# Optimization experiments

Measured on AMD Instinct MI355X. Metric: run time of the kernel, lower is better.

The kernel has to match this reference:

```python
import jax, jax.numpy as jnp
import numpy as np
import math

B, T, D_MODEL, H = 2, 2048, 768, 12
D = D_MODEL // H
EPS = 1e-8


def _l2norm(x, eps=EPS):
    # torch.nn.functional.normalize: x / max(||x||, eps)
    n = jnp.sqrt(jnp.sum(x * x, axis=-1, keepdims=True))
    return x / jnp.maximum(n, eps)


def setup_inputs() -> dict:
    key = jax.random.key(0)
    ks = jax.random.split(key, 7)
    sc = 1.0 / math.sqrt(D_MODEL)
    inp = {
        "query": jax.random.normal(ks[0], (B, T, D_MODEL), jnp.float32),
        "key": jax.random.normal(ks[1], (B, T, D_MODEL), jnp.float32),
        "value": jax.random.normal(ks[2], (B, T, D_MODEL), jnp.float32),
        "Wq": jax.random.normal(ks[3], (D_MODEL, D_MODEL), jnp.float32) * sc,
        "Wk": jax.random.normal(ks[4], (D_MODEL, D_MODEL), jnp.float32) * sc,
        "Wv": jax.random.normal(ks[5], (D_MODEL, D_MODEL), jnp.float32) * sc,
        "Wo": jax.random.normal(ks[6], (D_MODEL, D_MODEL), jnp.float32) * sc,
        "s_v": jnp.linspace(0.0, math.log(255.0), H).astype(jnp.float32),
        "s_r": jnp.zeros((H,), jnp.float32),
    }
    return inp


def reference(query, key, value, Wq, Wk, Wv, Wo, s_v, s_r):
    b, t, _ = query.shape

    def proj(x, W):  # Linear(bias=False) then split heads -> [B,H,T,D]
        return (x @ W.T).reshape(b, t, H, D).transpose(0, 2, 1, 3)

    q = _l2norm(proj(query, Wq))
    k = _l2norm(proj(key, Wk))
    v = _l2norm(proj(value, Wv))

    w = jnp.exp(s_v) + 1.0  # per-head decay exponent, in [2, 256]
    r = jnp.exp(s_r) + 1.0  # per-head scale

    # cosine-similarity scores in [-1, 1]
    s = jnp.einsum("bhqd,bhkd->bhqk", q, k)
    base = jnp.clip((s + 1.0) * 0.5, 0.0, 1.0)
    alpha = r[None, :, None, None] * jnp.power(base, w[None, :, None, None])

    # causal mask (no softmax normalization in screening attention)
    causal = jnp.tril(jnp.ones((t, t), dtype=bool))
    alpha = jnp.where(causal[None, None], alpha, 0.0)

    out = jnp.einsum("bhqk,bhkd->bhqd", alpha, v)  # [B,H,T,D]

    # TanhNorm: bound magnitude along head dim via tanh of the norm
    n = jnp.sqrt(jnp.sum(out * out, axis=-1, keepdims=True))
    out = jnp.tanh(n) * out / (n + EPS)

    out = out.transpose(0, 2, 1, 3).reshape(b, t, D_MODEL)
    return out @ Wo.T
```

## Files before the change

kernel.cpp:

```cpp
#include <hip/hip_runtime.h>
#include <hip/hip_bf16.h>
#include <math.h>


typedef __attribute__((ext_vector_type(8))) short short8;
typedef __attribute__((ext_vector_type(4))) float f32x4;
typedef __attribute__((ext_vector_type(4))) unsigned int uint4v;
typedef __attribute__((ext_vector_type(2))) unsigned int uint2v;
typedef __attribute__((ext_vector_type(4))) float float4v;

#define MFMA_BF16(a, b, c) __builtin_amdgcn_mfma_f32_16x16x32_bf16((a), (b), (c), 0, 0, 0)

static __device__ __forceinline__ unsigned short f2bf(float f) {
  union { float f; unsigned u; } v; v.f = f;
  unsigned r = v.u + 0x7FFFu + ((v.u >> 16) & 1u);
  return (unsigned short)(r >> 16);
}
static __device__ __forceinline__ unsigned pack2(float a, float b) {
  return (unsigned)f2bf(a) | ((unsigned)f2bf(b) << 16);
}
static __device__ __forceinline__ void gload_lds16(const void* g, void* l) {
  __builtin_amdgcn_global_load_lds((const __attribute__((address_space(1))) unsigned int*)g,
                                   (__attribute__((address_space(3))) unsigned int*)l, 16, 0, 0);
}

__global__ __launch_bounds__(256) void k_cvt(
    const float* __restrict__ s0, const float* __restrict__ s1, const float* __restrict__ s2,
    const float* __restrict__ s3, const float* __restrict__ s4, const float* __restrict__ s5,
    const float* __restrict__ s6, unsigned short* __restrict__ dst) {
  const size_t e = ((size_t)blockIdx.x * 256 + threadIdx.x) * 8;
  const float* src;
  size_t off;
  if (e < 9437184) {
    const int i = (int)(e / 3145728);
    src = (i == 0) ? s0 : (i == 1) ? s1 : s2;
    off = e - (size_t)i * 3145728;
  } else {
    const size_t ew = e - 9437184;
    const int i = (int)(ew / 589824);
    src = (i == 0) ? s3 : (i == 1) ? s4 : (i == 2) ? s5 : s6;
    off = ew - (size_t)i * 589824;
  }
  const float4v f0 = *(const float4v*)(src + off);
  const float4v f1 = *(const float4v*)(src + off + 4);
  uint4v u = {pack2(f0.x, f0.y), pack2(f0.z, f0.w), pack2(f1.x, f1.y), pack2(f1.z, f1.w)};
  *(uint4v*)(dst + e) = u;
}

__global__ __launch_bounds__(256) void k_proj(
    const unsigned short* __restrict__ Xb, const unsigned short* __restrict__ Wb,
    unsigned short* __restrict__ qb, unsigned short* __restrict__ kb,
    unsigned short* __restrict__ vtb) {
  __shared__ alignas(16) unsigned char smem[65536];
  float* o_s = (float*)smem;
  unsigned short* vt_s = (unsigned short*)smem;

  const int which = blockIdx.z;
  const unsigned short* X = Xb + (size_t)which * 3145728;
  const unsigned short* W = Wb + (size_t)which * 589824;

  const int mbase = blockIdx.x * 128;
  const int nb = blockIdx.y;
  const int tid = threadIdx.x;
  const int lane = tid & 63;
  const int wv = tid >> 6;
  const int wm = wv >> 1, wn = wv & 1;
  const int l15 = lane & 15, l4 = lane >> 4;

  const int srow8 = lane >> 3;
  const int schunk = (lane & 7) ^ srow8;

  f32x4 acc[4][4];
#pragma unroll
  for (int m = 0; m < 4; ++m)
#pragma unroll
    for (int n = 0; n < 4; ++n) acc[m][n] = (f32x4){0.f, 0.f, 0.f, 0.f};

#pragma unroll
  for (int i = 0; i < 4; ++i) {
    const int j = wv * 4 + i;
    gload_lds16(X + (size_t)(mbase + j * 8 + srow8) * 768 + schunk * 8, smem + j * 1024);
    gload_lds16(W + (size_t)(nb * 128 + j * 8 + srow8) * 768 + schunk * 8,
                smem + 16384 + j * 1024);
  }

  for (int ks = 0; ks < 12; ++ks) {
    const int cur = (ks & 1) * 32768;
    asm volatile("s_waitcnt vmcnt(0)" ::: "memory");
    __builtin_amdgcn_sched_barrier(0);
    __builtin_amdgcn_s_barrier();
    __builtin_amdgcn_sched_barrier(0);
    if (ks < 11) {
      const int nxt = ((ks + 1) & 1) * 32768;
      const int k0n = (ks + 1) * 64;
#pragma unroll
      for (int i = 0; i < 4; ++i) {
        const int j = wv * 4 + i;
        gload_lds16(X + (size_t)(mbase + j * 8 + srow8) * 768 + k0n + schunk * 8,
                    smem + nxt + j * 1024);
        gload_lds16(W + (size_t)(nb * 128 + j * 8 + srow8) * 768 + k0n + schunk * 8,
                    smem + nxt + 16384 + j * 1024);
      }
      __builtin_amdgcn_sched_barrier(0);
    }
    __builtin_amdgcn_s_setprio(1);
#pragma unroll
    for (int kc = 0; kc < 2; ++kc) {
      const int cx = (kc << 2) | l4;
      short8 ar[4], br[4];
#pragma unroll
      for (int m = 0; m < 4; ++m) {
        const int r = wm * 64 + m * 16 + l15;
        ar[m] = *(const short8*)(smem + cur + r * 128 + ((cx ^ (r & 7)) << 4));
      }
#pragma unroll
      for (int n = 0; n < 4; ++n) {
        const int r = wn * 64 + n * 16 + l15;
        br[n] = *(const short8*)(smem + cur + 16384 + r * 128 + ((cx ^ (r & 7)) << 4));
      }
#pragma unroll
      for (int m = 0; m < 4; ++m)
#pragma unroll
        for (int n = 0; n < 4; ++n) acc[m][n] = MFMA_BF16(ar[m], br[n], acc[m][n]);
    }
    __builtin_amdgcn_s_setprio(0);
  }

  const int b = mbase >> 11;
  const int tbase = mbase & 2047;
  const int row2 = tid >> 1, half = tid & 1;
  for (int p = 0; p < 2; ++p) {
    __syncthreads();
    if (wn == p) {
#pragma unroll
      for (int m = 0; m < 4; ++m)
#pragma unroll
        for (int n = 0; n < 4; ++n)
#pragma unroll
          for (int j = 0; j < 4; ++j)
            o_s[(wm * 64 + m * 16 + l4 * 4 + j) * 68 + n * 16 + l15] = acc[m][n][j];
    }
    __syncthreads();
    float v[32];
    float ss = 0.f;
#pragma unroll
    for (int c = 0; c < 8; ++c) {
      float4v f = *(const float4v*)(o_s + row2 * 68 + half * 32 + c * 4);
      v[c * 4 + 0] = f.x; v[c * 4 + 1] = f.y; v[c * 4 + 2] = f.z; v[c * 4 + 3] = f.w;
      ss += f.x * f.x + f.y * f.y + f.z * f.z + f.w * f.w;
    }
    ss += __shfl_xor(ss, 1);
    const float inv = 1.f / fmaxf(sqrtf(ss), 1e-8f);
    const int h = nb * 2 + p, bh = b * 12 + h;
    if (which < 2) {
      unsigned short* outp =
          ((which == 0) ? qb : kb) + ((size_t)bh * 2048 + tbase + row2) * 64 + half * 32;
#pragma unroll
      for (int c = 0; c < 4; ++c) {
        uint4v o = {pack2(v[c * 8 + 0] * inv, v[c * 8 + 1] * inv),
                    pack2(v[c * 8 + 2] * inv, v[c * 8 + 3] * inv),
                    pack2(v[c * 8 + 4] * inv, v[c * 8 + 5] * inv),
                    pack2(v[c * 8 + 6] * inv, v[c * 8 + 7] * inv)};
        *(uint4v*)(outp + c * 8) = o;
      }
      __syncthreads();
    } else {
      __syncthreads();
#pragma unroll
      for (int c = 0; c < 32; ++c)
        vt_s[(half * 32 + c) * 136 + row2] = f2bf(v[c] * inv);
      __syncthreads();
      const int d = tid >> 2, tc = (tid & 3) * 32;
      unsigned short* dst = vtb + ((size_t)bh * 64 + d) * 2048 + tbase + tc;
#pragma unroll
      for (int c = 0; c < 4; ++c)
        *(uint4v*)(dst + c * 8) = *(const uint4v*)(vt_s + d * 136 + tc + c * 8);
      __syncthreads();
    }
  }
}

__global__ __launch_bounds__(256) void k_attn(
    const unsigned short* __restrict__ qb, const unsigned short* __restrict__ kb,
    const unsigned short* __restrict__ vtb, const float* __restrict__ s_v,
    const float* __restrict__ s_r, unsigned short* __restrict__ attn) {
  __shared__ alignas(16) unsigned char smem[41984];
  unsigned short* p_s = (unsigned short*)(smem + 32768);
  float* o_s = (float*)smem;

  const int bid = blockIdx.x;
  const int ii = bid & 255, jj = bid >> 8;
  const int rank = (jj == 0) ? ii : (jj == 1) ? (511 - ii) : (512 + ii);
  const int qt = 31 - (rank / 24);
  const int bh = rank % 24;
  const int b = bh / 12, h = bh % 12;
  const int qbase = qt * 64;
  const unsigned short* Qp = qb + (size_t)bh * 2048 * 64;
  const unsigned short* Kp = kb + (size_t)bh * 2048 * 64;
  const unsigned short* VTp = vtb + (size_t)bh * 64 * 2048;

  const int tid = threadIdx.x;
  const int lane = tid & 63;
  const int wv = tid >> 6;
  const int wm = wv >> 1, wn = wv & 1;
  const int l15 = lane & 15, l4 = lane >> 4;
  const int srow8 = lane >> 3;
  const int schunk = (lane & 7) ^ srow8;

  const float w_h = expf(s_v[h]) + 1.0f;
  const float lr_h = log2f(expf(s_r[h]) + 1.0f);

#pragma unroll
  for (int i = 0; i < 2; ++i) {
    const int j = wv * 2 + i;
    gload_lds16(Kp + (size_t)(j * 8 + srow8) * 64 + schunk * 8, smem + j * 1024);
    gload_lds16(VTp + (size_t)(j * 8 + srow8) * 2048 + schunk * 8, smem + 16384 + j * 1024);
  }

  short8 qf[2][2];
#pragma unroll
  for (int n = 0; n < 2; ++n)
#pragma unroll
    for (int kc = 0; kc < 2; ++kc)
      qf[n][kc] = *(const short8*)(Qp + (size_t)(qbase + wn * 32 + n * 16 + l15) * 64 + kc * 32 +
                                   l4 * 8);

  f32x4 acc_o[2][2];
#pragma unroll
  for (int m = 0; m < 2; ++m)
#pragma unroll
    for (int n = 0; n < 2; ++n) acc_o[m][n] = (f32x4){0.f, 0.f, 0.f, 0.f};

  for (int kt = 0; kt <= qt; ++kt) {
    const int cur = (kt & 1) * 8192;
    asm volatile("s_waitcnt vmcnt(0)" ::: "memory");
    __builtin_amdgcn_sched_barrier(0);
    __builtin_amdgcn_s_barrier();
    __builtin_amdgcn_sched_barrier(0);
    if (kt < qt) {
      const int nxt = ((kt + 1) & 1) * 8192;
      const int kb2 = (kt + 1) * 64;
#pragma unroll
      for (int i = 0; i < 2; ++i) {
        const int j = wv * 2 + i;
        gload_lds16(Kp + (size_t)(kb2 + j * 8 + srow8) * 64 + schunk * 8, smem + nxt + j * 1024);
        gload_lds16(VTp + (size_t)(j * 8 + srow8) * 2048 + kb2 + schunk * 8,
                    smem + 16384 + nxt + j * 1024);
      }
      __builtin_amdgcn_sched_barrier(0);
    }
    f32x4 s_acc[2][2];
#pragma unroll
    for (int m = 0; m < 2; ++m)
#pragma unroll
      for (int n = 0; n < 2; ++n) s_acc[m][n] = (f32x4){0.f, 0.f, 0.f, 0.f};
    __builtin_amdgcn_s_setprio(1);
#pragma unroll
    for (int kc = 0; kc < 2; ++kc) {
      const int cx = (kc << 2) | l4;
      const int r0 = wm * 32 + l15, r1 = wm * 32 + 16 + l15;
      short8 a0 = *(const short8*)(smem + cur + r0 * 128 + ((cx ^ (r0 & 7)) << 4));
      short8 a1 = *(const short8*)(smem + cur + r1 * 128 + ((cx ^ (r1 & 7)) << 4));
      s_acc[0][0] = MFMA_BF16(a0, qf[0][kc], s_acc[0][0]);
      s_acc[0][1] = MFMA_BF16(a0, qf[1][kc], s_acc[0][1]);
      s_acc[1][0] = MFMA_BF16(a1, qf[0][kc], s_acc[1][0]);
      s_acc[1][1] = MFMA_BF16(a1, qf[1][kc], s_acc[1][1]);
    }
    __builtin_amdgcn_s_setprio(0);
    const bool diag = (kt == qt);
#pragma unroll
    for (int m = 0; m < 2; ++m)
#pragma unroll
      for (int n = 0; n < 2; ++n) {
        const int lkb = wm * 32 + m * 16 + l4 * 4;
        const int lq = wn * 32 + n * 16 + l15;
        float av[4];
#pragma unroll
        for (int t = 0; t < 4; ++t) {
          const float base = __builtin_amdgcn_fmed3f(fmaf(s_acc[m][n][t], 0.5f, 0.5f), 0.f, 1.f);
          float a = __builtin_amdgcn_exp2f(fmaf(w_h, __builtin_amdgcn_logf(base), lr_h));
          if (diag && (lkb + t) > lq) a = 0.f;
          av[t] = a;
        }
        uint2v u = {pack2(av[0], av[1]), pack2(av[2], av[3])};
        *(uint2v*)(p_s + lq * 72 + lkb) = u;
      }
    asm volatile("s_waitcnt lgkmcnt(0)" ::: "memory");
    __builtin_amdgcn_sched_barrier(0);
    __builtin_amdgcn_s_barrier();
    __builtin_amdgcn_sched_barrier(0);
    __builtin_amdgcn_s_setprio(1);
#pragma unroll
    for (int kc = 0; kc < 2; ++kc) {
      const int cx = (kc << 2) | l4;
      const int r0 = wm * 32 + l15, r1 = wm * 32 + 16 + l15;
      short8 pa0 = *(const short8*)(p_s + (wn * 32 + l15) * 72 + kc * 32 + l4 * 8);
      short8 pa1 = *(const short8*)(p_s + (wn * 32 + 16 + l15) * 72 + kc * 32 + l4 * 8);
      short8 vb0 = *(const short8*)(smem + 16384 + cur + r0 * 128 + ((cx ^ (r0 & 7)) << 4));
      short8 vb1 = *(const short8*)(smem + 16384 + cur + r1 * 128 + ((cx ^ (r1 & 7)) << 4));
      acc_o[0][0] = MFMA_BF16(pa0, vb0, acc_o[0][0]);
      acc_o[0][1] = MFMA_BF16(pa0, vb1, acc_o[0][1]);
      acc_o[1][0] = MFMA_BF16(pa1, vb0, acc_o[1][0]);
      acc_o[1][1] = MFMA_BF16(pa1, vb1, acc_o[1][1]);
    }
    __builtin_amdgcn_s_setprio(0);
  }
  __syncthreads();
#pragma unroll
  for (int qi = 0; qi < 2; ++qi)
#pragma unroll
    for (int di = 0; di < 2; ++di)
#pragma unroll
      for (int j = 0; j < 4; ++j)
        o_s[(wn * 32 + qi * 16 + l4 * 4 + j) * 68 + wm * 32 + di * 16 + l15] = acc_o[qi][di][j];
  __syncthreads();
  {
    const int row = tid >> 2, q4 = tid & 3;
    float vals[16];
    float ss = 0.f;
#pragma unroll
    for (int j = 0; j < 16; ++j) {
      vals[j] = o_s[row * 68 + q4 * 16 + j];
      ss += vals[j] * vals[j];
    }
    ss += __shfl_xor(ss, 1);
    ss += __shfl_xor(ss, 2);
    const float nrm = sqrtf(ss);
    const float sc = tanhf(nrm) / (nrm + 1e-8f);
    unsigned short* dst = attn + (size_t)(b * 2048 + qbase + row) * 768 + h * 64 + q4 * 16;
    uint4v o0 = {pack2(vals[0] * sc, vals[1] * sc), pack2(vals[2] * sc, vals[3] * sc),
                 pack2(vals[4] * sc, vals[5] * sc), pack2(vals[6] * sc, vals[7] * sc)};
    uint4v o1 = {pack2(vals[8] * sc, vals[9] * sc), pack2(vals[10] * sc, vals[11] * sc),
                 pack2(vals[12] * sc, vals[13] * sc), pack2(vals[14] * sc, vals[15] * sc)};
    *(uint4v*)(dst) = o0;
    *(uint4v*)(dst + 8) = o1;
  }
}

__global__ __launch_bounds__(256) void k_outproj(const unsigned short* __restrict__ attn,
                                                 const unsigned short* __restrict__ Wob,
                                                 float* __restrict__ out) {
  __shared__ alignas(16) unsigned char smem[65536];
  const int mbase = blockIdx.x * 128;
  const int nb = blockIdx.y;
  const int tid = threadIdx.x;
  const int lane = tid & 63;
  const int wv = tid >> 6;
  const int wm = wv >> 1, wn = wv & 1;
  const int l15 = lane & 15, l4 = lane >> 4;
  const int srow8 = lane >> 3;
  const int schunk = (lane & 7) ^ srow8;

  f32x4 acc[4][4];
#pragma unroll
  for (int m = 0; m < 4; ++m)
#pragma unroll
    for (int n = 0; n < 4; ++n) acc[m][n] = (f32x4){0.f, 0.f, 0.f, 0.f};

#pragma unroll
  for (int i = 0; i < 4; ++i) {
    const int j = wv * 4 + i;
    gload_lds16(attn + (size_t)(mbase + j * 8 + srow8) * 768 + schunk * 8, smem + j * 1024);
    gload_lds16(Wob + (size_t)(nb * 128 + j * 8 + srow8) * 768 + schunk * 8,
                smem + 16384 + j * 1024);
  }

  for (int ks = 0; ks < 12; ++ks) {
    const int cur = (ks & 1) * 32768;
    asm volatile("s_waitcnt vmcnt(0)" ::: "memory");
    __builtin_amdgcn_sched_barrier(0);
    __builtin_amdgcn_s_barrier();
    __builtin_amdgcn_sched_barrier(0);
    if (ks < 11) {
      const int nxt = ((ks + 1) & 1) * 32768;
      const int k0n = (ks + 1) * 64;
#pragma unroll
      for (int i = 0; i < 4; ++i) {
        const int j = wv * 4 + i;
        gload_lds16(attn + (size_t)(mbase + j * 8 + srow8) * 768 + k0n + schunk * 8,
                    smem + nxt + j * 1024);
        gload_lds16(Wob + (size_t)(nb * 128 + j * 8 + srow8) * 768 + k0n + schunk * 8,
                    smem + nxt + 16384 + j * 1024);
      }
      __builtin_amdgcn_sched_barrier(0);
    }
    __builtin_amdgcn_s_setprio(1);
#pragma unroll
    for (int kc = 0; kc < 2; ++kc) {
      const int cx = (kc << 2) | l4;
      short8 ar[4], br[4];
#pragma unroll
      for (int m = 0; m < 4; ++m) {
        const int r = wm * 64 + m * 16 + l15;
        ar[m] = *(const short8*)(smem + cur + r * 128 + ((cx ^ (r & 7)) << 4));
      }
#pragma unroll
      for (int n = 0; n < 4; ++n) {
        const int r = wn * 64 + n * 16 + l15;
        br[n] = *(const short8*)(smem + cur + 16384 + r * 128 + ((cx ^ (r & 7)) << 4));
      }
#pragma unroll
      for (int m = 0; m < 4; ++m)
#pragma unroll
        for (int n = 0; n < 4; ++n) acc[m][n] = MFMA_BF16(ar[m], br[n], acc[m][n]);
    }
    __builtin_amdgcn_s_setprio(0);
  }
#pragma unroll
  for (int m = 0; m < 4; ++m)
#pragma unroll
    for (int n = 0; n < 4; ++n)
#pragma unroll
      for (int j = 0; j < 4; ++j)
        out[(size_t)(mbase + wm * 64 + m * 16 + l4 * 4 + j) * 768 + nb * 128 + wn * 64 + n * 16 +
            l15] = acc[m][n][j];
}

extern "C" void kernel_launch(void* const* d_in, const int* in_sizes, int n_in, void* d_out,
                              int out_size, void* d_ws, size_t ws_size, hipStream_t stream) {
  (void)in_sizes;
  (void)n_in;
  (void)out_size;
  (void)ws_size;
  const float* query = (const float*)d_in[0];
  const float* key = (const float*)d_in[1];
  const float* value = (const float*)d_in[2];
  const float* Wq = (const float*)d_in[3];
  const float* Wk = (const float*)d_in[4];
  const float* Wv = (const float*)d_in[5];
  const float* Wo = (const float*)d_in[6];
  const float* s_v = (const float*)d_in[7];
  const float* s_r = (const float*)d_in[8];
  float* out = (float*)d_out;

  unsigned short* cvt = (unsigned short*)d_ws;
  unsigned short* Xb = cvt;
  unsigned short* Wb = cvt + 9437184;
  unsigned short* qb = cvt + 11796480;
  unsigned short* kb = qb + 3145728;
  unsigned short* vtb = kb + 3145728;
  unsigned short* attn = cvt;

  k_cvt<<<5760, 256, 0, stream>>>(query, key, value, Wq, Wk, Wv, Wo, cvt);
  k_proj<<<dim3(32, 6, 3), 256, 0, stream>>>(Xb, Wb, qb, kb, vtb);
  k_attn<<<dim3(768), 256, 0, stream>>>(qb, kb, vtb, s_v, s_r, attn);
  k_outproj<<<dim3(32, 6), 256, 0, stream>>>(attn, Wb + 3 * 589824, out);
}
```

Before: 89.53 us.

## Fuse fp32-to-bf16 activation conversion into projection GEMM A-tile loads

Stops converting the query/key/value activations in a separate pass. The projection kernel now loads the fp32 activations into registers, packs them to bf16 and writes them into the swizzled LDS tile, while the weights still arrive through async global-to-LDS loads. This removes a full write and read of the bf16 activation copy and shrinks the conversion kernel to weights only. In exchange it adds register pressure, ALU packing work and an LDS store plus lgkmcnt wait on the GEMM critical path, and each output-column block re-reads twice the activation bytes from global memory.

```diff
diff --git a/kernel.cpp b/kernel.cpp
--- a/kernel.cpp
+++ b/kernel.cpp
@@ -24,23 +24,13 @@
                                    (__attribute__((address_space(3))) unsigned int*)l, 16, 0, 0);
 }
 
-__global__ __launch_bounds__(256) void k_cvt(
-    const float* __restrict__ s0, const float* __restrict__ s1, const float* __restrict__ s2,
+__global__ __launch_bounds__(256) void k_cvtW(
     const float* __restrict__ s3, const float* __restrict__ s4, const float* __restrict__ s5,
     const float* __restrict__ s6, unsigned short* __restrict__ dst) {
   const size_t e = ((size_t)blockIdx.x * 256 + threadIdx.x) * 8;
-  const float* src;
-  size_t off;
-  if (e < 9437184) {
-    const int i = (int)(e / 3145728);
-    src = (i == 0) ? s0 : (i == 1) ? s1 : s2;
-    off = e - (size_t)i * 3145728;
-  } else {
-    const size_t ew = e - 9437184;
-    const int i = (int)(ew / 589824);
-    src = (i == 0) ? s3 : (i == 1) ? s4 : (i == 2) ? s5 : s6;
-    off = ew - (size_t)i * 589824;
-  }
+  const int i = (int)(e / 589824);
+  const float* src = (i == 0) ? s3 : (i == 1) ? s4 : (i == 2) ? s5 : s6;
+  const size_t off = e - (size_t)i * 589824;
   const float4v f0 = *(const float4v*)(src + off);
   const float4v f1 = *(const float4v*)(src + off + 4);
   uint4v u = {pack2(f0.x, f0.y), pack2(f0.z, f0.w), pack2(f1.x, f1.y), pack2(f1.z, f1.w)};
@@ -48,15 +38,15 @@
 }
 
 __global__ __launch_bounds__(256) void k_proj(
-    const unsigned short* __restrict__ Xb, const unsigned short* __restrict__ Wb,
-    unsigned short* __restrict__ qb, unsigned short* __restrict__ kb,
-    unsigned short* __restrict__ vtb) {
+    const float* __restrict__ Xq, const float* __restrict__ Xk, const float* __restrict__ Xv,
+    const unsigned short* __restrict__ Wb, unsigned short* __restrict__ qb,
+    unsigned short* __restrict__ kb, unsigned short* __restrict__ vtb) {
   __shared__ alignas(16) unsigned char smem[65536];
   float* o_s = (float*)smem;
   unsigned short* vt_s = (unsigned short*)smem;
 
   const int which = blockIdx.z;
-  const unsigned short* X = Xb + (size_t)which * 3145728;
+  const float* X = (which == 0) ? Xq : (which == 1) ? Xk : Xv;
   const unsigned short* W = Wb + (size_t)which * 589824;
 
   const int mbase = blockIdx.x * 128;
@@ -76,10 +66,21 @@
 #pragma unroll
     for (int n = 0; n < 4; ++n) acc[m][n] = (f32x4){0.f, 0.f, 0.f, 0.f};
 
+  const float* asrc[4];
+#pragma unroll
+  for (int i = 0; i < 4; ++i)
+    asrc[i] = X + (size_t)(mbase + (wv * 4 + i) * 8 + srow8) * 768 + schunk * 8;
+
+  float4v af[4][2];
+
+#pragma unroll
+  for (int i = 0; i < 4; ++i) {
+    af[i][0] = *(const float4v*)(asrc[i]);
+    af[i][1] = *(const float4v*)(asrc[i] + 4);
+  }
 #pragma unroll
   for (int i = 0; i < 4; ++i) {
     const int j = wv * 4 + i;
-    gload_lds16(X + (size_t)(mbase + j * 8 + srow8) * 768 + schunk * 8, smem + j * 1024);
     gload_lds16(W + (size_t)(nb * 128 + j * 8 + srow8) * 768 + schunk * 8,
                 smem + 16384 + j * 1024);
   }
@@ -88,16 +89,28 @@
     const int cur = (ks & 1) * 32768;
     asm volatile("s_waitcnt vmcnt(0)" ::: "memory");
     __builtin_amdgcn_sched_barrier(0);
+#pragma unroll
+    for (int i = 0; i < 4; ++i) {
+      uint4v u = {pack2(af[i][0].x, af[i][0].y), pack2(af[i][0].z, af[i][0].w),
+                  pack2(af[i][1].x, af[i][1].y), pack2(af[i][1].z, af[i][1].w)};
+      *(uint4v*)(smem + cur + (wv * 4 + i) * 1024 + lane * 16) = u;
+    }
+    __builtin_amdgcn_sched_barrier(0);
+    asm volatile("s_waitcnt lgkmcnt(0)" ::: "memory");
+    __builtin_amdgcn_sched_barrier(0);
     __builtin_amdgcn_s_barrier();
     __builtin_amdgcn_sched_barrier(0);
     if (ks < 11) {
+      const int k0n = (ks + 1) * 64;
       const int nxt = ((ks + 1) & 1) * 32768;
-      const int k0n = (ks + 1) * 64;
+#pragma unroll
+      for (int i = 0; i < 4; ++i) {
+        af[i][0] = *(const float4v*)(asrc[i] + k0n);
+        af[i][1] = *(const float4v*)(asrc[i] + k0n + 4);
+      }
 #pragma unroll
       for (int i = 0; i < 4; ++i) {
         const int j = wv * 4 + i;
-        gload_lds16(X + (size_t)(mbase + j * 8 + srow8) * 768 + k0n + schunk * 8,
-                    smem + nxt + j * 1024);
         gload_lds16(W + (size_t)(nb * 128 + j * 8 + srow8) * 768 + k0n + schunk * 8,
                     smem + nxt + 16384 + j * 1024);
       }
@@ -433,16 +446,14 @@
   const float* s_r = (const float*)d_in[8];
   float* out = (float*)d_out;
 
-  unsigned short* cvt = (unsigned short*)d_ws;
-  unsigned short* Xb = cvt;
-  unsigned short* Wb = cvt + 9437184;
-  unsigned short* qb = cvt + 11796480;
+  unsigned short* Wb = (unsigned short*)d_ws;
+  unsigned short* qb = Wb + 2359296;
   unsigned short* kb = qb + 3145728;
   unsigned short* vtb = kb + 3145728;
-  unsigned short* attn = cvt;
-
-  k_cvt<<<5760, 256, 0, stream>>>(query, key, value, Wq, Wk, Wv, Wo, cvt);
-  k_proj<<<dim3(32, 6, 3), 256, 0, stream>>>(Xb, Wb, qb, kb, vtb);
+  unsigned short* attn = vtb + 3145728;
+
+  k_cvtW<<<1152, 256, 0, stream>>>(Wq, Wk, Wv, Wo, Wb);
+  k_proj<<<dim3(32, 6, 3), 256, 0, stream>>>(query, key, value, Wb, qb, kb, vtb);
   k_attn<<<dim3(768), 256, 0, stream>>>(qb, kb, vtb, s_v, s_r, attn);
   k_outproj<<<dim3(32, 6), 256, 0, stream>>>(attn, Wb + 3 * 589824, out);
 }
```

Result: slower. 91.78 us (+2.5%).

## Stream-K split of causal attention tiles with partial sums and separate tanh-norm kernel

Applied to the files above, without the earlier changes.

Flattens all (head, query-tile, key-tile) causal work items into a linear sequence and gives each of the 768 blocks an equal contiguous strip of 16 or 17 tiles. A strip can cross query-tile and head boundaries, so each block writes fp32 partial accumulators into per-slot buffers instead of finishing rows itself. A new reduction kernel sums the partials, applies the TanhNorm and writes bf16 output. This targets load imbalance from triangular causal work, at the cost of extra fp32 partial traffic, an extra launch, and re-loading Q fragments at row changes.

```diff
diff --git a/kernel.cpp b/kernel.cpp
--- a/kernel.cpp
+++ b/kernel.cpp
@@ -22,6 +22,12 @@
 static __device__ __forceinline__ void gload_lds16(const void* g, void* l) {
   __builtin_amdgcn_global_load_lds((const __attribute__((address_space(1))) unsigned int*)g,
                                    (__attribute__((address_space(3))) unsigned int*)l, 16, 0, 0);
+}
+static __device__ __forceinline__ int strip_first(int s) {
+  return (s < 384) ? s * 17 : 6528 + (s - 384) * 16;
+}
+static __device__ __forceinline__ int strip_of(int g) {
+  return (g < 6528) ? g / 17 : 384 + (g - 6528) / 16;
 }
 
 __global__ __launch_bounds__(256) void k_cvt(
@@ -66,7 +72,6 @@
   const int wv = tid >> 6;
   const int wm = wv >> 1, wn = wv & 1;
   const int l15 = lane & 15, l4 = lane >> 4;
-
   const int srow8 = lane >> 3;
   const int schunk = (lane & 7) ^ srow8;
 
@@ -183,21 +188,20 @@
 __global__ __launch_bounds__(256) void k_attn(
     const unsigned short* __restrict__ qb, const unsigned short* __restrict__ kb,
     const unsigned short* __restrict__ vtb, const float* __restrict__ s_v,
-    const float* __restrict__ s_r, unsigned short* __restrict__ attn) {
+    const float* __restrict__ s_r, float* __restrict__ partials) {
   __shared__ alignas(16) unsigned char smem[41984];
   unsigned short* p_s = (unsigned short*)(smem + 32768);
-  float* o_s = (float*)smem;
-
-  const int bid = blockIdx.x;
-  const int ii = bid & 255, jj = bid >> 8;
-  const int rank = (jj == 0) ? ii : (jj == 1) ? (511 - ii) : (512 + ii);
-  const int qt = 31 - (rank / 24);
-  const int bh = rank % 24;
-  const int b = bh / 12, h = bh % 12;
-  const int qbase = qt * 64;
-  const unsigned short* Qp = qb + (size_t)bh * 2048 * 64;
-  const unsigned short* Kp = kb + (size_t)bh * 2048 * 64;
-  const unsigned short* VTp = vtb + (size_t)bh * 64 * 2048;
+
+  const int s = blockIdx.x;
+  const int gs = strip_first(s);
+  const int ge = strip_first(s + 1);
+
+  int bh = gs / 528;
+  int ii = gs - bh * 528;
+  int qt = (int)((sqrtf(8.f * (float)ii + 1.f) - 1.f) * 0.5f);
+  while ((qt + 1) * (qt + 2) / 2 <= ii) ++qt;
+  while (qt * (qt + 1) / 2 > ii) --qt;
+  int kt = ii - qt * (qt + 1) / 2;
 
   const int tid = threadIdx.x;
   const int lane = tid & 63;
@@ -207,23 +211,32 @@
   const int srow8 = lane >> 3;
   const int schunk = (lane & 7) ^ srow8;
 
-  const float w_h = expf(s_v[h]) + 1.0f;
-  const float lr_h = log2f(expf(s_r[h]) + 1.0f);
-
-#pragma unroll
-  for (int i = 0; i < 2; ++i) {
-    const int j = wv * 2 + i;
-    gload_lds16(Kp + (size_t)(j * 8 + srow8) * 64 + schunk * 8, smem + j * 1024);
-    gload_lds16(VTp + (size_t)(j * 8 + srow8) * 2048 + schunk * 8, smem + 16384 + j * 1024);
-  }
-
+  {
+    const unsigned short* Kp = kb + (size_t)bh * 131072;
+    const unsigned short* VTp = vtb + (size_t)bh * 131072;
+    const int kbase = kt * 64;
+#pragma unroll
+    for (int i = 0; i < 2; ++i) {
+      const int j = wv * 2 + i;
+      gload_lds16(Kp + (size_t)(kbase + j * 8 + srow8) * 64 + schunk * 8, smem + j * 1024);
+      gload_lds16(VTp + (size_t)(j * 8 + srow8) * 2048 + kbase + schunk * 8,
+                  smem + 16384 + j * 1024);
+    }
+  }
+
+  float w_h = expf(s_v[bh % 12]) + 1.0f;
+  float lr_h = log2f(expf(s_r[bh % 12]) + 1.0f);
   short8 qf[2][2];
-#pragma unroll
-  for (int n = 0; n < 2; ++n)
-#pragma unroll
-    for (int kc = 0; kc < 2; ++kc)
-      qf[n][kc] = *(const short8*)(Qp + (size_t)(qbase + wn * 32 + n * 16 + l15) * 64 + kc * 32 +
-                                   l4 * 8);
+  {
+    const unsigned short* Qp = qb + (size_t)bh * 131072;
+    const int qbase = qt * 64;
+#pragma unroll
+    for (int n = 0; n < 2; ++n)
+#pragma unroll
+      for (int kc = 0; kc < 2; ++kc)
+        qf[n][kc] = *(const short8*)(Qp + (size_t)(qbase + wn * 32 + n * 16 + l15) * 64 +
+                                     kc * 32 + l4 * 8);
+  }
 
   f32x4 acc_o[2][2];
 #pragma unroll
@@ -231,20 +244,29 @@
 #pragma unroll
     for (int n = 0; n < 2; ++n) acc_o[m][n] = (f32x4){0.f, 0.f, 0.f, 0.f};
 
-  for (int kt = 0; kt <= qt; ++kt) {
-    const int cur = (kt & 1) * 8192;
+  for (int g = gs; g < ge; ++g) {
+    const int cur = ((g - gs) & 1) * 8192;
+    const int qbase = qt * 64;
     asm volatile("s_waitcnt vmcnt(0)" ::: "memory");
     __builtin_amdgcn_sched_barrier(0);
     __builtin_amdgcn_s_barrier();
     __builtin_amdgcn_sched_barrier(0);
-    if (kt < qt) {
-      const int nxt = ((kt + 1) & 1) * 8192;
-      const int kb2 = (kt + 1) * 64;
+    int bh2 = bh, qt2 = qt, kt2 = kt + 1;
+    if (kt2 > qt2) {
+      kt2 = 0;
+      ++qt2;
+      if (qt2 == 32) { qt2 = 0; ++bh2; }
+    }
+    if (g + 1 < ge) {
+      const int nxt = ((g + 1 - gs) & 1) * 8192;
+      const unsigned short* Kp2 = kb + (size_t)bh2 * 131072;
+      const unsigned short* VTp2 = vtb + (size_t)bh2 * 131072;
+      const int kb2 = kt2 * 64;
 #pragma unroll
       for (int i = 0; i < 2; ++i) {
         const int j = wv * 2 + i;
-        gload_lds16(Kp + (size_t)(kb2 + j * 8 + srow8) * 64 + schunk * 8, smem + nxt + j * 1024);
-        gload_lds16(VTp + (size_t)(j * 8 + srow8) * 2048 + kb2 + schunk * 8,
+        gload_lds16(Kp2 + (size_t)(kb2 + j * 8 + srow8) * 64 + schunk * 8, smem + nxt + j * 1024);
+        gload_lds16(VTp2 + (size_t)(j * 8 + srow8) * 2048 + kb2 + schunk * 8,
                     smem + 16384 + nxt + j * 1024);
       }
       __builtin_amdgcn_sched_barrier(0);
@@ -304,37 +326,80 @@
       acc_o[1][1] = MFMA_BF16(pa1, vb1, acc_o[1][1]);
     }
     __builtin_amdgcn_s_setprio(0);
-  }
-  __syncthreads();
-#pragma unroll
-  for (int qi = 0; qi < 2; ++qi)
-#pragma unroll
-    for (int di = 0; di < 2; ++di)
-#pragma unroll
-      for (int j = 0; j < 4; ++j)
-        o_s[(wn * 32 + qi * 16 + l4 * 4 + j) * 68 + wm * 32 + di * 16 + l15] = acc_o[qi][di][j];
-  __syncthreads();
-  {
-    const int row = tid >> 2, q4 = tid & 3;
-    float vals[16];
-    float ss = 0.f;
-#pragma unroll
-    for (int j = 0; j < 16; ++j) {
-      vals[j] = o_s[row * 68 + q4 * 16 + j];
-      ss += vals[j] * vals[j];
-    }
-    ss += __shfl_xor(ss, 1);
-    ss += __shfl_xor(ss, 2);
-    const float nrm = sqrtf(ss);
-    const float sc = tanhf(nrm) / (nrm + 1e-8f);
-    unsigned short* dst = attn + (size_t)(b * 2048 + qbase + row) * 768 + h * 64 + q4 * 16;
-    uint4v o0 = {pack2(vals[0] * sc, vals[1] * sc), pack2(vals[2] * sc, vals[3] * sc),
-                 pack2(vals[4] * sc, vals[5] * sc), pack2(vals[6] * sc, vals[7] * sc)};
-    uint4v o1 = {pack2(vals[8] * sc, vals[9] * sc), pack2(vals[10] * sc, vals[11] * sc),
-                 pack2(vals[12] * sc, vals[13] * sc), pack2(vals[14] * sc, vals[15] * sc)};
-    *(uint4v*)(dst) = o0;
-    *(uint4v*)(dst + 8) = o1;
-  }
+    if (diag || (g + 1 == ge)) {
+      const int g0 = bh * 528 + qt * (qt + 1) / 2;
+      const int slot = s - strip_of(g0);
+      float* pb = partials + (((size_t)slot * 24 + bh) * 2048 + qbase) * 64;
+#pragma unroll
+      for (int qi = 0; qi < 2; ++qi)
+#pragma unroll
+        for (int di = 0; di < 2; ++di)
+#pragma unroll
+          for (int j = 0; j < 4; ++j)
+            pb[(size_t)(wn * 32 + qi * 16 + l4 * 4 + j) * 64 + wm * 32 + di * 16 + l15] =
+                acc_o[qi][di][j];
+#pragma unroll
+      for (int m = 0; m < 2; ++m)
+#pragma unroll
+        for (int n = 0; n < 2; ++n) acc_o[m][n] = (f32x4){0.f, 0.f, 0.f, 0.f};
+      if (g + 1 < ge) {
+        if (bh2 != bh) {
+          w_h = expf(s_v[bh2 % 12]) + 1.0f;
+          lr_h = log2f(expf(s_r[bh2 % 12]) + 1.0f);
+        }
+        const unsigned short* Qp2 = qb + (size_t)bh2 * 131072;
+        const int qbase2 = qt2 * 64;
+#pragma unroll
+        for (int n = 0; n < 2; ++n)
+#pragma unroll
+          for (int kc = 0; kc < 2; ++kc)
+            qf[n][kc] = *(const short8*)(Qp2 + (size_t)(qbase2 + wn * 32 + n * 16 + l15) * 64 +
+                                         kc * 32 + l4 * 8);
+      }
+    }
+    bh = bh2; qt = qt2; kt = kt2;
+  }
+}
+
+__global__ __launch_bounds__(256) void k_tanh(const float* __restrict__ partials,
+                                              unsigned short* __restrict__ attn) {
+  const int tid = threadIdx.x;
+  const int rg = blockIdx.x * 64 + (tid >> 2);
+  const int q4 = tid & 3;
+  const int bh = rg >> 11, t = rg & 2047;
+  const int qt = t >> 6;
+  const int g0 = bh * 528 + qt * (qt + 1) / 2;
+  const int cnt = strip_of(g0 + qt) - strip_of(g0) + 1;
+  float v[16];
+  const float* b0 = partials + ((size_t)bh * 2048 + t) * 64 + q4 * 16;
+#pragma unroll
+  for (int c = 0; c < 4; ++c) {
+    float4v f = *(const float4v*)(b0 + c * 4);
+    v[c * 4 + 0] = f.x; v[c * 4 + 1] = f.y; v[c * 4 + 2] = f.z; v[c * 4 + 3] = f.w;
+  }
+  for (int p = 1; p < cnt; ++p) {
+    const float* bp = b0 + (size_t)p * 3145728;
+#pragma unroll
+    for (int c = 0; c < 4; ++c) {
+      float4v f = *(const float4v*)(bp + c * 4);
+      v[c * 4 + 0] += f.x; v[c * 4 + 1] += f.y; v[c * 4 + 2] += f.z; v[c * 4 + 3] += f.w;
+    }
+  }
+  float ss = 0.f;
+#pragma unroll
+  for (int j = 0; j < 16; ++j) ss += v[j] * v[j];
+  ss += __shfl_xor(ss, 1);
+  ss += __shfl_xor(ss, 2);
+  const float nrm = sqrtf(ss);
+  const float sc = tanhf(nrm) / (nrm + 1e-8f);
+  unsigned short* dst =
+      attn + ((size_t)((bh / 12) * 2048 + t)) * 768 + (bh % 12) * 64 + q4 * 16;
+  uint4v o0 = {pack2(v[0] * sc, v[1] * sc), pack2(v[2] * sc, v[3] * sc),
+               pack2(v[4] * sc, v[5] * sc), pack2(v[6] * sc, v[7] * sc)};
+  uint4v o1 = {pack2(v[8] * sc, v[9] * sc), pack2(v[10] * sc, v[11] * sc),
+               pack2(v[12] * sc, v[13] * sc), pack2(v[14] * sc, v[15] * sc)};
+  *(uint4v*)(dst) = o0;
+  *(uint4v*)(dst + 8) = o1;
 }
 
 __global__ __launch_bounds__(256) void k_outproj(const unsigned short* __restrict__ attn,
@@ -439,10 +504,12 @@
   unsigned short* qb = cvt + 11796480;
   unsigned short* kb = qb + 3145728;
   unsigned short* vtb = kb + 3145728;
+  float* partials = (float*)(cvt + 21233664);
   unsigned short* attn = cvt;
 
   k_cvt<<<5760, 256, 0, stream>>>(query, key, value, Wq, Wk, Wv, Wo, cvt);
   k_proj<<<dim3(32, 6, 3), 256, 0, stream>>>(Xb, Wb, qb, kb, vtb);
-  k_attn<<<dim3(768), 256, 0, stream>>>(qb, kb, vtb, s_v, s_r, attn);
+  k_attn<<<dim3(768), 256, 0, stream>>>(qb, kb, vtb, s_v, s_r, partials);
+  k_tanh<<<dim3(768), 256, 0, stream>>>(partials, attn);
   k_outproj<<<dim3(32, 6), 256, 0, stream>>>(attn, Wb + 3 * 589824, out);
 }
```

New measurement: 103.4 us. +15.5%, slower.
